# Performance work log

Measured on AMD Instinct MI355X. Metric: run time of the kernel, lower is better.

Reference implementation:

```python
import jax, jax.numpy as jnp
import numpy as np

N_HEADS = 16


def setup_inputs() -> dict:
    key = jax.random.key(0)
    k1, k2, k3, k4 = jax.random.split(key, 4)
    B, T, C = 2, 2048, 1024
    x = jax.random.normal(k1, (B, T, C), dtype=jnp.float32)
    scale = 1.0 / np.sqrt(C)
    Wq = jax.random.normal(k2, (C, C), dtype=jnp.float32) * scale
    Wk = jax.random.normal(k3, (C, C), dtype=jnp.float32) * scale
    Wv = jax.random.normal(k4, (C, C), dtype=jnp.float32) * scale
    return {"x": x, "Wq": Wq, "Wk": Wk, "Wv": Wv}


def reference(x, Wq, Wk, Wv):
    B, T, C = x.shape
    H = N_HEADS
    Dh = C // H
    # Faithful to original: direct view of (B,T,C) -> (B,H,T,Dh) (no transpose)
    q = (x @ Wq.T).reshape(B, H, T, Dh)
    k = (x @ Wk.T).reshape(B, H, T, Dh)
    v = (x @ Wv.T).reshape(B, H, T, Dh)
    scores = jnp.einsum('bhqd,bhkd->bhqk', q, k) * (1.0 / (Dh ** 0.5))
    mask = jnp.tril(jnp.ones((T, T), dtype=bool))  # causal mask
    scores = jnp.where(mask, scores, -jnp.inf)
    att = jax.nn.softmax(scores, axis=-1)
    out = jnp.einsum('bhqk,bhkd->bhqd', att, v)
    return out.reshape(B, T, C)
```

## Files before the change

kernel.cpp:

```cpp
#include <hip/hip_runtime.h>
#include <hip/hip_bf16.h>
#include <stdint.h>

#define AS1 __attribute__((address_space(1)))
#define AS3 __attribute__((address_space(3)))

typedef __bf16 bf16x8 __attribute__((ext_vector_type(8)));
typedef float  f32x4  __attribute__((ext_vector_type(4)));
typedef unsigned short ushort8v __attribute__((ext_vector_type(8)));
typedef unsigned short ushort4v __attribute__((ext_vector_type(4)));
typedef short short8v __attribute__((ext_vector_type(8)));
typedef short short4v __attribute__((ext_vector_type(4)));

__device__ __forceinline__ unsigned short f2bf(float f) {
    unsigned int u = __float_as_uint(f);
    u += 0x7fffu + ((u >> 16) & 1u);
    return (unsigned short)(u >> 16);
}
__device__ __forceinline__ unsigned int pk2bf(float a, float b) {
    __hip_bfloat162 h = __float22bfloat162_rn(make_float2(a, b));
    unsigned int u;
    __builtin_memcpy(&u, &h, 4);
    return u;
}
__device__ __forceinline__ void g2lds16(const void* gp, void* lp) {
    __builtin_amdgcn_global_load_lds((AS1 void*)gp, (AS3 void*)lp, 16, 0, 0);
}
#define E2(x) __builtin_amdgcn_exp2f(x)

__global__ __launch_bounds__(256) void cast_all(const float* __restrict__ x,
                                                const float* __restrict__ w0,
                                                const float* __restrict__ w1,
                                                const float* __restrict__ w2,
                                                unsigned short* __restrict__ xb,
                                                unsigned short* __restrict__ wc) {
    int id = blockIdx.x;
    const float* s;
    unsigned short* d;
    int base;
    if (id < 4096) { s = x; d = xb; base = id; }
    else {
        int z = (id - 4096) >> 10;
        s = (z == 0) ? w0 : (z == 1) ? w1 : w2;
        d = wc + (size_t)z * 1048576;
        base = (id - 4096) & 1023;
    }
    int i = (base * 256 + threadIdx.x) * 4;
    float4 v = *(const float4*)(s + i);
    ushort4v o = { f2bf(v.x), f2bf(v.y), f2bf(v.z), f2bf(v.w) };
    *(ushort4v*)(d + i) = o;
}

__global__ __launch_bounds__(256) void gemm_qkv(const unsigned short* __restrict__ X,
                                                const unsigned short* __restrict__ W,
                                                unsigned short* __restrict__ QKV) {
    const int K = 1024, N = 1024;
    const int z = blockIdx.z;
    const unsigned short* A = X;
    const unsigned short* B = W + (size_t)z * (1024 * 1024);
    unsigned short* C = QKV + (size_t)z * (4096 * 1024);
    const float qs = (z == 0) ? 0.18033688011112042f : 1.0f;

    const int m0 = blockIdx.y * 128;
    const int n0 = blockIdx.x * 128;

    __shared__ unsigned short As[128 * 32];
    __shared__ unsigned short Bs[128 * 32];

    const int t = threadIdx.x;
    const int w = t >> 6;
    const int l = t & 63;
    const int wm = (w >> 1) * 64;
    const int wn = (w & 1) * 64;
    const int cl = l & 15;
    const int quad = l >> 4;

    const int srow = w * 16 + (l >> 2);
    const int scol = (l & 3) * 8;

    f32x4 acc[4][4] = {};

    for (int k0 = 0; k0 < K; k0 += 32) {
        g2lds16(A + (size_t)(m0 + srow) * K + k0 + scol,      As + w * 512);
        g2lds16(A + (size_t)(m0 + 64 + srow) * K + k0 + scol, As + 2048 + w * 512);
        g2lds16(B + (size_t)(n0 + srow) * K + k0 + scol,      Bs + w * 512);
        g2lds16(B + (size_t)(n0 + 64 + srow) * K + k0 + scol, Bs + 2048 + w * 512);
        __syncthreads();

        bf16x8 af[4], bfr[4];
        #pragma unroll
        for (int i = 0; i < 4; ++i)
            af[i] = *(const bf16x8*)(As + (wm + i * 16 + cl) * 32 + quad * 8);
        #pragma unroll
        for (int j = 0; j < 4; ++j)
            bfr[j] = *(const bf16x8*)(Bs + (wn + j * 16 + cl) * 32 + quad * 8);
        #pragma unroll
        for (int i = 0; i < 4; ++i)
            #pragma unroll
            for (int j = 0; j < 4; ++j)
                acc[i][j] = __builtin_amdgcn_mfma_f32_16x16x32_bf16(af[i], bfr[j], acc[i][j], 0, 0, 0);
        __syncthreads();
    }

    #pragma unroll
    for (int i = 0; i < 4; ++i) {
        #pragma unroll
        for (int r = 0; r < 4; ++r) {
            size_t row = (size_t)(m0 + wm + i * 16 + quad * 4 + r);
            #pragma unroll
            for (int j = 0; j < 4; ++j)
                C[row * N + (n0 + wn + j * 16 + cl)] = f2bf(acc[i][j][r] * qs);
        }
    }
}

__global__ __launch_bounds__(256) void vtrans(const unsigned short* __restrict__ Vn,
                                              unsigned short* __restrict__ V3) {
    const int bh = blockIdx.y;
    const int T0 = blockIdx.x * 128;
    __shared__ unsigned short L[128 * 72];
    const int t = threadIdx.x;

    const unsigned short* src = Vn + (size_t)bh * 131072 + (size_t)T0 * 64;
    #pragma unroll
    for (int p = 0; p < 4; ++p) {
        int r = p * 32 + (t >> 3), c = (t & 7) * 8;
        *(ushort8v*)(L + r * 72 + c) = *(const ushort8v*)(src + (size_t)r * 64 + c);
    }
    __syncthreads();
    unsigned short* dst = V3 + (size_t)bh * 131072 + (size_t)(T0 >> 4) * 1024;
    #pragma unroll
    for (int p = 0; p < 2; ++p) {
        int item = p * 256 + t;
        int kb = item >> 6, cl = (item >> 2) & 15, qk = item & 3;
        ushort8v a, b;
        #pragma unroll
        for (int u = 0; u < 8; ++u) {
            int dt = u >> 2, j = u & 3;
            a[u] = L[(kb * 16 + qk * 4 + j) * 72 + dt * 16 + cl];
            b[u] = L[(kb * 16 + qk * 4 + j) * 72 + (dt + 2) * 16 + cl];
        }
        unsigned short* dp = dst + kb * 1024 + cl * 64 + qk * 16;
        *(ushort8v*)(dp) = a;
        *(ushort8v*)(dp + 8) = b;
    }
}

__global__ __launch_bounds__(256, 4) void attn(const unsigned short* __restrict__ QK,
                                               const unsigned short* __restrict__ V3,
                                               float* __restrict__ Out) {
    const int id = blockIdx.x;
    const int bh = id & 31;
    const int bb = 31 - (id >> 5);
    const int t = threadIdx.x;
    const int w = t >> 6;
    const int l = t & 63;
    const int cl = l & 15;
    const int quad = l >> 4;
    const int c7 = cl & 7;

    const size_t bhoff = (size_t)bh * 131072;
    const unsigned short* Qb = QK + bhoff;
    const unsigned short* Kb = QK + (size_t)4194304 + bhoff;
    const unsigned short* Vb = V3 + bhoff;
    float* Ob = Out + bhoff;

    __shared__ unsigned short KVs[2][8192];

    const int g2 = t + 256;
    const int kO1 = (t >> 3) * 64 + (((t & 7) ^ ((t >> 3) & 7)) * 8);
    const int kO2 = (g2 >> 3) * 64 + (((g2 & 7) ^ ((g2 >> 3) & 7)) * 8);
    const int wg1 = t & 63;
    const int wg2 = g2 & 63;
    const int vO1 = (t >> 6) * 512 + ((wg1 ^ ((wg1 >> 3) & 7)) * 8);
    const int vO2 = (g2 >> 6) * 512 + ((wg2 ^ ((wg2 >> 3) & 7)) * 8);
    const int lB1 = w * 512;
    const int lB2 = 2048 + w * 512;

    const int oK0 = cl * 64 + (((quad)     ^ c7) * 8);
    const int oK1 = cl * 64 + (((quad + 4) ^ c7) * 8);
    const int oV0 = cl * 64 + (((quad * 2)     ^ c7) * 8);
    const int oV1 = cl * 64 + (((quad * 2 + 1) ^ c7) * 8);

    const int mrel = w * 16 + cl;
    const int nch = bb + 1;
    const int m0w = bb * 64 + w * 16;

    bf16x8 qf0, qf1;
    {
        const unsigned short* qa = Qb + (size_t)(m0w + cl) * 64 + quad * 8;
        qf0 = *(const bf16x8*)(qa);
        qf1 = *(const bf16x8*)(qa + 32);
    }

    f32x4 o[4] = {};
    float lps = 0.f;

    {
        unsigned short* s = &KVs[0][0];
        g2lds16(Kb + kO1, s + lB1);
        g2lds16(Kb + kO2, s + lB2);
        g2lds16(Vb + vO1, s + 4096 + lB1);
        g2lds16(Vb + vO2, s + 4096 + lB2);
    }

    for (int c = 0; c < nch; ++c) {
        __syncthreads();
        if (c + 1 < nch) {
            unsigned short* s = &KVs[(c + 1) & 1][0];
            const size_t off = (size_t)(c + 1) * 4096;
            g2lds16(Kb + off + kO1, s + lB1);
            g2lds16(Kb + off + kO2, s + lB2);
            g2lds16(Vb + off + vO1, s + 4096 + lB1);
            g2lds16(Vb + off + vO2, s + 4096 + lB2);
        }
        const unsigned short* Kl = &KVs[c & 1][0];
        const unsigned short* Vl = Kl + 4096;
        const bool masked = (c == bb);

        bf16x8 kf0[4], kf1[4];
        #pragma unroll
        for (int kt = 0; kt < 4; ++kt) {
            kf0[kt] = *(const bf16x8*)(Kl + kt * 1024 + oK0);
            kf1[kt] = *(const bf16x8*)(Kl + kt * 1024 + oK1);
        }
        f32x4 st[4] = {};
        __builtin_amdgcn_s_setprio(1);
        #pragma unroll
        for (int kt = 0; kt < 4; ++kt) {
            st[kt] = __builtin_amdgcn_mfma_f32_16x16x32_bf16(kf0[kt], qf0, st[kt], 0, 0, 0);
            st[kt] = __builtin_amdgcn_mfma_f32_16x16x32_bf16(kf1[kt], qf1, st[kt], 0, 0, 0);
        }
        __builtin_amdgcn_s_setprio(0);

        short4v pb[4];
        #pragma unroll
        for (int kt = 0; kt < 4; ++kt) {
            float p0, p1, p2, p3;
            if (masked) {
                const int lk = kt * 16 + quad * 4;
                p0 = (lk     <= mrel) ? E2(st[kt][0]) : 0.f;
                p1 = (lk + 1 <= mrel) ? E2(st[kt][1]) : 0.f;
                p2 = (lk + 2 <= mrel) ? E2(st[kt][2]) : 0.f;
                p3 = (lk + 3 <= mrel) ? E2(st[kt][3]) : 0.f;
            } else {
                p0 = E2(st[kt][0]);
                p1 = E2(st[kt][1]);
                p2 = E2(st[kt][2]);
                p3 = E2(st[kt][3]);
            }
            lps += (p0 + p1) + (p2 + p3);
            uint2 u = { pk2bf(p0, p1), pk2bf(p2, p3) };
            short4v pv;
            __builtin_memcpy(&pv, &u, 8);
            pb[kt] = pv;
        }

        __builtin_amdgcn_s_setprio(1);
        #pragma unroll
        for (int kt = 0; kt < 4; ++kt) {
            short8v v0 = *(const short8v*)(Vl + kt * 1024 + oV0);
            short8v v1 = *(const short8v*)(Vl + kt * 1024 + oV1);
            short4v a0 = __builtin_shufflevector(v0, v0, 0, 1, 2, 3);
            short4v a1 = __builtin_shufflevector(v0, v0, 4, 5, 6, 7);
            short4v a2 = __builtin_shufflevector(v1, v1, 0, 1, 2, 3);
            short4v a3 = __builtin_shufflevector(v1, v1, 4, 5, 6, 7);
            o[0] = __builtin_amdgcn_mfma_f32_16x16x16bf16_1k(a0, pb[kt], o[0], 0, 0, 0);
            o[1] = __builtin_amdgcn_mfma_f32_16x16x16bf16_1k(a1, pb[kt], o[1], 0, 0, 0);
            o[2] = __builtin_amdgcn_mfma_f32_16x16x16bf16_1k(a2, pb[kt], o[2], 0, 0, 0);
            o[3] = __builtin_amdgcn_mfma_f32_16x16x16bf16_1k(a3, pb[kt], o[3], 0, 0, 0);
        }
        __builtin_amdgcn_s_setprio(0);
    }

    lps += __shfl_xor(lps, 16);
    lps += __shfl_xor(lps, 32);
    const float inv = 1.0f / lps;
    #pragma unroll
    for (int dt = 0; dt < 4; ++dt) {
        f32x4 r = o[dt];
        r[0] *= inv; r[1] *= inv; r[2] *= inv; r[3] *= inv;
        *(f32x4*)(Ob + (size_t)(m0w + cl) * 64 + dt * 16 + quad * 4) = r;
    }
}

extern "C" void kernel_launch(void* const* d_in, const int* in_sizes, int n_in,
                              void* d_out, int out_size, void* d_ws, size_t ws_size,
                              hipStream_t stream) {
    const float* x  = (const float*)d_in[0];
    const float* Wq = (const float*)d_in[1];
    const float* Wk = (const float*)d_in[2];
    const float* Wv = (const float*)d_in[3];
    float* out = (float*)d_out;

    unsigned short* xb  = (unsigned short*)d_ws;
    unsigned short* wc  = xb + (size_t)4096 * 1024;
    unsigned short* qkv = wc + (size_t)3 * 1024 * 1024;
    unsigned short* vt  = qkv + (size_t)3 * 4096 * 1024;

    hipLaunchKernelGGL(cast_all, dim3(7168), dim3(256), 0, stream, x, Wq, Wk, Wv, xb, wc);
    hipLaunchKernelGGL(gemm_qkv, dim3(8, 32, 3), dim3(256), 0, stream, xb, wc, qkv);
    hipLaunchKernelGGL(vtrans, dim3(16, 32), dim3(256), 0, stream, qkv + (size_t)2 * 4096 * 1024, vt);
    hipLaunchKernelGGL(attn, dim3(1024), dim3(256), 0, stream, qkv, vt, out);
}
```

Before: 147.4 us.

## Fuse V transpose into QKV GEMM epilogue and remap blocks per XCD

The separate vtrans kernel is removed. The V projection blocks now scatter their results straight into the transposed, MFMA-friendly V layout from the GEMM epilogue, which saves one kernel launch and a full read and write of V. The GEMM grid also becomes a flat 1D launch whose block index is decoded so that blocks on the same XCD share M and N tiles, aiming for better L2 reuse. The cost is that the V epilogue writes scattered 2-byte elements with poor coalescing.

```diff
diff --git a/kernel.cpp b/kernel.cpp
--- a/kernel.cpp
+++ b/kernel.cpp
@@ -53,16 +53,23 @@
 
 __global__ __launch_bounds__(256) void gemm_qkv(const unsigned short* __restrict__ X,
                                                 const unsigned short* __restrict__ W,
-                                                unsigned short* __restrict__ QKV) {
+                                                unsigned short* __restrict__ QKV,
+                                                unsigned short* __restrict__ VT) {
     const int K = 1024, N = 1024;
-    const int z = blockIdx.z;
+    const int b = blockIdx.x;
+    const int xcd = b & 7;
+    const int s = b >> 3;
+    const int ml = s / 12;
+    const int r12 = s - ml * 12;
+    const int z = r12 >> 2;
+    const int nl = r12 & 3;
+    const int m0 = (ml * 4 + (xcd >> 1)) * 128;
+    const int n0 = ((xcd & 1) * 4 + nl) * 128;
+
     const unsigned short* A = X;
     const unsigned short* B = W + (size_t)z * (1024 * 1024);
     unsigned short* C = QKV + (size_t)z * (4096 * 1024);
     const float qs = (z == 0) ? 0.18033688011112042f : 1.0f;
-
-    const int m0 = blockIdx.y * 128;
-    const int n0 = blockIdx.x * 128;
 
     __shared__ unsigned short As[128 * 32];
     __shared__ unsigned short Bs[128 * 32];
@@ -102,47 +109,36 @@
         __syncthreads();
     }
 
-    #pragma unroll
-    for (int i = 0; i < 4; ++i) {
-        #pragma unroll
-        for (int r = 0; r < 4; ++r) {
-            size_t row = (size_t)(m0 + wm + i * 16 + quad * 4 + r);
+    if (z == 2) {
+        #pragma unroll
+        for (int i = 0; i < 4; ++i) {
             #pragma unroll
-            for (int j = 0; j < 4; ++j)
-                C[row * N + (n0 + wn + j * 16 + cl)] = f2bf(acc[i][j][r] * qs);
-        }
-    }
-}
-
-__global__ __launch_bounds__(256) void vtrans(const unsigned short* __restrict__ Vn,
-                                              unsigned short* __restrict__ V3) {
-    const int bh = blockIdx.y;
-    const int T0 = blockIdx.x * 128;
-    __shared__ unsigned short L[128 * 72];
-    const int t = threadIdx.x;
-
-    const unsigned short* src = Vn + (size_t)bh * 131072 + (size_t)T0 * 64;
-    #pragma unroll
-    for (int p = 0; p < 4; ++p) {
-        int r = p * 32 + (t >> 3), c = (t & 7) * 8;
-        *(ushort8v*)(L + r * 72 + c) = *(const ushort8v*)(src + (size_t)r * 64 + c);
-    }
-    __syncthreads();
-    unsigned short* dst = V3 + (size_t)bh * 131072 + (size_t)(T0 >> 4) * 1024;
-    #pragma unroll
-    for (int p = 0; p < 2; ++p) {
-        int item = p * 256 + t;
-        int kb = item >> 6, cl = (item >> 2) & 15, qk = item & 3;
-        ushort8v a, b;
-        #pragma unroll
-        for (int u = 0; u < 8; ++u) {
-            int dt = u >> 2, j = u & 3;
-            a[u] = L[(kb * 16 + qk * 4 + j) * 72 + dt * 16 + cl];
-            b[u] = L[(kb * 16 + qk * 4 + j) * 72 + (dt + 2) * 16 + cl];
-        }
-        unsigned short* dp = dst + kb * 1024 + cl * 64 + qk * 16;
-        *(ushort8v*)(dp) = a;
-        *(ushort8v*)(dp + 8) = b;
+            for (int r = 0; r < 4; ++r) {
+                int row = m0 + wm + i * 16 + quad * 4 + r;
+                size_t rb = (size_t)(row >> 7) * 131072 + (size_t)(row & 127) * 1024;
+                #pragma unroll
+                for (int j = 0; j < 4; ++j) {
+                    int col = n0 + wn + j * 16 + cl;
+                    int c6 = col >> 6;
+                    size_t a = rb + (size_t)(col & 15) * 64
+                             + (size_t)((c6 >> 2) & 3) * 16
+                             + (size_t)((col >> 4) & 3) * 4
+                             + (size_t)(c6 & 3);
+                    VT[a] = f2bf(acc[i][j][r]);
+                }
+            }
+        }
+    } else {
+        #pragma unroll
+        for (int i = 0; i < 4; ++i) {
+            #pragma unroll
+            for (int r = 0; r < 4; ++r) {
+                size_t row = (size_t)(m0 + wm + i * 16 + quad * 4 + r);
+                #pragma unroll
+                for (int j = 0; j < 4; ++j)
+                    C[row * N + (n0 + wn + j * 16 + cl)] = f2bf(acc[i][j][r] * qs);
+            }
+        }
     }
 }
 
@@ -299,7 +295,6 @@
     unsigned short* vt  = qkv + (size_t)3 * 4096 * 1024;
 
     hipLaunchKernelGGL(cast_all, dim3(7168), dim3(256), 0, stream, x, Wq, Wk, Wv, xb, wc);
-    hipLaunchKernelGGL(gemm_qkv, dim3(8, 32, 3), dim3(256), 0, stream, xb, wc, qkv);
-    hipLaunchKernelGGL(vtrans, dim3(16, 32), dim3(256), 0, stream, qkv + (size_t)2 * 4096 * 1024, vt);
+    hipLaunchKernelGGL(gemm_qkv, dim3(768), dim3(256), 0, stream, xb, wc, qkv, vt);
     hipLaunchKernelGGL(attn, dim3(1024), dim3(256), 0, stream, qkv, vt, out);
 }
```

Result: slower. 169.9 us (+15.2%).

## Restructure QKV GEMM into 256x256 double-buffered tiles with XOR-swizzled LDS

Applied to the files above, without the earlier changes.

Rewrites the QKV projection GEMM to use 512-thread blocks computing 256x256 output tiles with K-step 64. The next K-slab is double-buffered in LDS and prefetched during the MFMA phases, with split barriers and partial vmcnt waits. LDS columns are XOR-swizzled to avoid bank conflicts, and MFMA sections run at raised wave priority. The aim is to hide global-load latency and raise arithmetic intensity. The cost is much more LDS and registers per block and a grid of only 192 blocks, which may underfill the GPU's CUs.

```diff
diff --git a/kernel.cpp b/kernel.cpp
--- a/kernel.cpp
+++ b/kernel.cpp
@@ -51,65 +51,101 @@
     *(ushort4v*)(d + i) = o;
 }
 
-__global__ __launch_bounds__(256) void gemm_qkv(const unsigned short* __restrict__ X,
-                                                const unsigned short* __restrict__ W,
-                                                unsigned short* __restrict__ QKV) {
+#define VMW(n) asm volatile("s_waitcnt vmcnt(" #n ")" ::: "memory")
+#define NOW
+#define PH(I, S, CUR, STG, ENDW) do {                                          \
+    const int kx_ = ((S) * 32 + quad * 8) ^ ((cl & 4) << 2);                   \
+    bf16x8 af_[4], bq_[4];                                                     \
+    _Pragma("unroll")                                                          \
+    for (int m_ = 0; m_ < 4; ++m_)                                             \
+        af_[m_] = *(const bf16x8*)&SA[CUR][((w >> 2) * 128 + ((I) * 4 + m_) * 16 + cl) * 64 + kx_]; \
+    _Pragma("unroll")                                                          \
+    for (int n_ = 0; n_ < 4; ++n_)                                             \
+        bq_[n_] = *(const bf16x8*)&SB[CUR][((w & 3) * 64 + n_ * 16 + cl) * 64 + kx_]; \
+    STG;                                                                       \
+    __builtin_amdgcn_s_barrier();                                              \
+    asm volatile("s_waitcnt lgkmcnt(0)" ::: "memory");                         \
+    __builtin_amdgcn_sched_barrier(0);                                         \
+    __builtin_amdgcn_s_setprio(1);                                             \
+    _Pragma("unroll")                                                          \
+    for (int m_ = 0; m_ < 4; ++m_)                                             \
+        _Pragma("unroll")                                                      \
+        for (int n_ = 0; n_ < 4; ++n_)                                         \
+            acc[(I) * 4 + m_][n_] = __builtin_amdgcn_mfma_f32_16x16x32_bf16(   \
+                af_[m_], bq_[n_], acc[(I) * 4 + m_][n_], 0, 0, 0);             \
+    __builtin_amdgcn_s_setprio(0);                                             \
+    __builtin_amdgcn_sched_barrier(0);                                         \
+    ENDW;                                                                      \
+    __builtin_amdgcn_s_barrier();                                              \
+} while (0)
+
+__global__ __launch_bounds__(512, 2) void gemm_qkv(const unsigned short* __restrict__ X,
+                                                   const unsigned short* __restrict__ W,
+                                                   unsigned short* __restrict__ QKV) {
     const int K = 1024, N = 1024;
-    const int z = blockIdx.z;
+    const int b = blockIdx.x;
+    const int z = b >> 6;
+    const int r = b & 63;
+    const int m0 = (r >> 2) * 256;
+    const int n0 = (r & 3) * 256;
+
     const unsigned short* A = X;
-    const unsigned short* B = W + (size_t)z * (1024 * 1024);
+    const unsigned short* Bp = W + (size_t)z * (1024 * 1024);
     unsigned short* C = QKV + (size_t)z * (4096 * 1024);
     const float qs = (z == 0) ? 0.18033688011112042f : 1.0f;
 
-    const int m0 = blockIdx.y * 128;
-    const int n0 = blockIdx.x * 128;
-
-    __shared__ unsigned short As[128 * 32];
-    __shared__ unsigned short Bs[128 * 32];
+    __shared__ unsigned short SA[2][16384];
+    __shared__ unsigned short SB[2][16384];
 
     const int t = threadIdx.x;
     const int w = t >> 6;
     const int l = t & 63;
-    const int wm = (w >> 1) * 64;
-    const int wn = (w & 1) * 64;
     const int cl = l & 15;
     const int quad = l >> 4;
 
-    const int srow = w * 16 + (l >> 2);
-    const int scol = (l & 3) * 8;
-
-    f32x4 acc[4][4] = {};
-
-    for (int k0 = 0; k0 < K; k0 += 32) {
-        g2lds16(A + (size_t)(m0 + srow) * K + k0 + scol,      As + w * 512);
-        g2lds16(A + (size_t)(m0 + 64 + srow) * K + k0 + scol, As + 2048 + w * 512);
-        g2lds16(B + (size_t)(n0 + srow) * K + k0 + scol,      Bs + w * 512);
-        g2lds16(B + (size_t)(n0 + 64 + srow) * K + k0 + scol, Bs + 2048 + w * 512);
-        __syncthreads();
-
-        bf16x8 af[4], bfr[4];
-        #pragma unroll
-        for (int i = 0; i < 4; ++i)
-            af[i] = *(const bf16x8*)(As + (wm + i * 16 + cl) * 32 + quad * 8);
-        #pragma unroll
-        for (int j = 0; j < 4; ++j)
-            bfr[j] = *(const bf16x8*)(Bs + (wn + j * 16 + cl) * 32 + quad * 8);
-        #pragma unroll
-        for (int i = 0; i < 4; ++i)
+    const int srow8 = t >> 3;
+    const int klog = ((t & 7) * 8) ^ (((t >> 5) & 1) << 4);
+    const unsigned short* Abase = A + (size_t)(m0 + srow8) * K + klog;
+    const unsigned short* Bbase = Bp + (size_t)(n0 + srow8) * K + klog;
+    unsigned short* const sa0 = &SA[0][w * 512];
+    unsigned short* const sa1 = &SA[1][w * 512];
+    unsigned short* const sb0 = &SB[0][w * 512];
+    unsigned short* const sb1 = &SB[1][w * 512];
+
+    f32x4 acc[8][4] = {};
+
+#define STGA(nb, q, k0) g2lds16(Abase + (size_t)(q) * 65536 + (k0), ((nb) ? sa1 : sa0) + (q) * 4096)
+#define STGB(nb, q, k0) g2lds16(Bbase + (size_t)(q) * 65536 + (k0), ((nb) ? sb1 : sb0) + (q) * 4096)
+
+    STGB(0, 0, 0); STGB(0, 1, 0); STGB(0, 2, 0); STGB(0, 3, 0);
+    STGA(0, 0, 0); STGA(0, 2, 0); STGA(0, 1, 0); STGA(0, 3, 0);
+    VMW(2);
+    __builtin_amdgcn_s_barrier();
+
+    for (int tt = 0; tt < 15; ++tt) {
+        const int cur = tt & 1, nxt = cur ^ 1;
+        const int k1 = (tt + 1) * 64;
+        PH(0, 0, cur, { STGB(nxt, 0, k1); STGB(nxt, 1, k1); }, NOW);
+        PH(0, 1, cur, { STGB(nxt, 2, k1); STGB(nxt, 3, k1); }, VMW(4));
+        PH(1, 0, cur, { STGA(nxt, 0, k1); STGA(nxt, 2, k1); }, NOW);
+        PH(1, 1, cur, { STGA(nxt, 1, k1); STGA(nxt, 3, k1); }, VMW(2));
+    }
+    PH(0, 0, 1, {}, NOW);
+    PH(0, 1, 1, {}, VMW(0));
+    PH(1, 0, 1, {}, NOW);
+    PH(1, 1, 1, {}, NOW);
+
+#undef STGA
+#undef STGB
+
+    #pragma unroll
+    for (int mf = 0; mf < 8; ++mf) {
+        #pragma unroll
+        for (int rr = 0; rr < 4; ++rr) {
+            size_t row = (size_t)(m0 + (w >> 2) * 128 + mf * 16 + quad * 4 + rr);
             #pragma unroll
-            for (int j = 0; j < 4; ++j)
-                acc[i][j] = __builtin_amdgcn_mfma_f32_16x16x32_bf16(af[i], bfr[j], acc[i][j], 0, 0, 0);
-        __syncthreads();
-    }
-
-    #pragma unroll
-    for (int i = 0; i < 4; ++i) {
-        #pragma unroll
-        for (int r = 0; r < 4; ++r) {
-            size_t row = (size_t)(m0 + wm + i * 16 + quad * 4 + r);
-            #pragma unroll
-            for (int j = 0; j < 4; ++j)
-                C[row * N + (n0 + wn + j * 16 + cl)] = f2bf(acc[i][j][r] * qs);
+            for (int nf = 0; nf < 4; ++nf)
+                C[row * N + (n0 + (w & 3) * 64 + nf * 16 + cl)] = f2bf(acc[mf][nf][rr] * qs);
         }
     }
 }
@@ -299,7 +335,7 @@
     unsigned short* vt  = qkv + (size_t)3 * 4096 * 1024;
 
     hipLaunchKernelGGL(cast_all, dim3(7168), dim3(256), 0, stream, x, Wq, Wk, Wv, xb, wc);
-    hipLaunchKernelGGL(gemm_qkv, dim3(8, 32, 3), dim3(256), 0, stream, xb, wc, qkv);
+    hipLaunchKernelGGL(gemm_qkv, dim3(192), dim3(512), 0, stream, xb, wc, qkv);
     hipLaunchKernelGGL(vtrans, dim3(16, 32), dim3(256), 0, stream, qkv + (size_t)2 * 4096 * 1024, vt);
     hipLaunchKernelGGL(attn, dim3(1024), dim3(256), 0, stream, qkv, vt, out);
 }
```

After: 150.3 us. About the same (+1.9%).
